# Kernel optimization log

Measured on AMD Instinct MI355X. Metric: run time of the kernel, lower is better.

Reference implementation:

```python
import jax, jax.numpy as jnp
import numpy as np

B, S, D_IN, D_OUT = 4, 2048, 1024, 1024

def setup_inputs() -> dict:
    key = jax.random.key(0)
    k_x, k_q, k_k, k_v = jax.random.split(key, 4)
    return {
        "x": jax.random.normal(k_x, (B, S, D_IN), dtype=jnp.float32),
        "W_query": jax.random.uniform(k_q, (D_IN, D_OUT), dtype=jnp.float32),
        "W_key": jax.random.uniform(k_k, (D_IN, D_OUT), dtype=jnp.float32),
        "W_value": jax.random.uniform(k_v, (D_IN, D_OUT), dtype=jnp.float32),
    }

def reference(x, W_query, W_key, W_value):
    seq_len = x.shape[1]
    d_out = W_key.shape[-1]
    # fused QKV projection: x @ concat([Wq, Wk, Wv], -1), then split
    qkv = x @ jnp.concatenate([W_query, W_key, W_value], axis=-1)  # [B,S,3*d_out]
    query, key, value = jnp.split(qkv, 3, axis=2)
    # raw scores [B,S,S]; causal mask applied BEFORE scaling (as in source)
    attn_weights = jnp.einsum("bqd,bkd->bqk", query, key)
    causal = jnp.triu(jnp.ones((seq_len, seq_len), dtype=bool), k=1)
    attn_weights = jnp.where(causal[None, :, :], -jnp.inf, attn_weights)
    scaled = attn_weights / jnp.asarray(d_out, x.dtype) ** 0.5
    attn_scores = jax.nn.softmax(scaled, axis=-1)  # dropout p=0 -> identity
    context_vectors = jnp.einsum("bqk,bkd->bqd", attn_scores, value)
    return (context_vectors, attn_scores)
```

## Files before the change

kernel.cpp:

```cpp
#include <hip/hip_runtime.h>
#include <cstdint>
#include <cstddef>


#define S_LEN 2048
#define D_DIM 1024
#define NBATCH 4
#define MEG (1024 * 1024)

typedef __attribute__((ext_vector_type(4))) float floatx4;
typedef __attribute__((ext_vector_type(8))) __bf16 bf16x8;
typedef __attribute__((ext_vector_type(8))) short short8v;

__device__ __forceinline__ unsigned short f2bf(float f) {
  union { float f; unsigned u; } v; v.f = f;
  unsigned r = v.u + 0x7FFF + ((v.u >> 16) & 1);
  return (unsigned short)(r >> 16);
}
__device__ __forceinline__ float bf2f(unsigned short h) {
  union { unsigned u; float f; } v; v.u = ((unsigned)h) << 16; return v.f;
}

__device__ __forceinline__ void async_copy16(const void* g, void* l) {
  __builtin_amdgcn_global_load_lds(
      (const __attribute__((address_space(1))) void*)g,
      (__attribute__((address_space(3))) void*)l, 16, 0, 0);
}

__device__ __forceinline__ void gemm_bt_core(
    const short* __restrict__ A, const short* __restrict__ B,
    int lda, int ldb, int kIters, int blockM, int blockN,
    short (*As)[32], short (*Bs)[32], floatx4 (&acc)[4][4])
{
  const int tid  = threadIdx.x;
  const int lane = tid & 63;
  const int wave = tid >> 6;
  const int wm = (wave >> 1) * 64;
  const int wn = (wave & 1) * 64;
  const int fm = lane & 15;
  const int fk = (lane >> 4) * 8;
  const int r0 = tid >> 2;
  const int c0 = (tid & 3) * 8;

  floatx4 zero = {0.f, 0.f, 0.f, 0.f};
  #pragma unroll
  for (int i = 0; i < 4; ++i)
    #pragma unroll
    for (int j = 0; j < 4; ++j)
      acc[i][j] = zero;

  const short* a0 = A + (size_t)(blockM + r0) * lda + c0;
  const short* a1 = a0 + (size_t)64 * lda;
  const short* b0 = B + (size_t)(blockN + r0) * ldb + c0;
  const short* b1 = b0 + (size_t)64 * ldb;
  short* as0 = &As[r0][c0];
  short* as1 = &As[r0 + 64][c0];
  short* bs0 = &Bs[r0][c0];
  short* bs1 = &Bs[r0 + 64][c0];

  for (int kt = 0; kt < kIters; ++kt) {
    const int kb = kt * 32;
    async_copy16(a0 + kb, as0);
    async_copy16(a1 + kb, as1);
    async_copy16(b0 + kb, bs0);
    async_copy16(b1 + kb, bs1);
    __syncthreads();
    bf16x8 af[4], bfr[4];
    #pragma unroll
    for (int i = 0; i < 4; ++i)
      af[i] = *(const bf16x8*)(&As[wm + i * 16 + fm][fk]);
    #pragma unroll
    for (int j = 0; j < 4; ++j)
      bfr[j] = *(const bf16x8*)(&Bs[wn + j * 16 + fm][fk]);
    #pragma unroll
    for (int i = 0; i < 4; ++i)
      #pragma unroll
      for (int j = 0; j < 4; ++j)
        acc[i][j] = __builtin_amdgcn_mfma_f32_16x16x32_bf16(af[i], bfr[j], acc[i][j], 0, 0, 0);
    __syncthreads();
  }
}

__device__ __forceinline__ void gemm_bt_split_core(
    const short* __restrict__ Ah, const short* __restrict__ Al,
    const short* __restrict__ Bh, const short* __restrict__ Bl,
    int lda, int ldb, int kIters, int blockM, int blockN,
    short (*AsH)[32], short (*AsL)[32], short (*BsH)[32], short (*BsL)[32],
    floatx4 (&acc)[4][4])
{
  const int tid  = threadIdx.x;
  const int lane = tid & 63;
  const int wave = tid >> 6;
  const int wm = (wave >> 1) * 64;
  const int wn = (wave & 1) * 64;
  const int fm = lane & 15;
  const int fk = (lane >> 4) * 8;
  const int r0 = tid >> 2;
  const int c0 = (tid & 3) * 8;

  floatx4 zero = {0.f, 0.f, 0.f, 0.f};
  #pragma unroll
  for (int i = 0; i < 4; ++i)
    #pragma unroll
    for (int j = 0; j < 4; ++j)
      acc[i][j] = zero;

  const size_t oa0 = (size_t)(blockM + r0) * lda + c0;
  const size_t oa1 = oa0 + (size_t)64 * lda;
  const size_t ob0 = (size_t)(blockN + r0) * ldb + c0;
  const size_t ob1 = ob0 + (size_t)64 * ldb;
  short* lah0 = &AsH[r0][c0]; short* lah1 = &AsH[r0 + 64][c0];
  short* lal0 = &AsL[r0][c0]; short* lal1 = &AsL[r0 + 64][c0];
  short* lbh0 = &BsH[r0][c0]; short* lbh1 = &BsH[r0 + 64][c0];
  short* lbl0 = &BsL[r0][c0]; short* lbl1 = &BsL[r0 + 64][c0];

  for (int kt = 0; kt < kIters; ++kt) {
    const int kb = kt * 32;
    async_copy16(Ah + oa0 + kb, lah0);
    async_copy16(Ah + oa1 + kb, lah1);
    async_copy16(Al + oa0 + kb, lal0);
    async_copy16(Al + oa1 + kb, lal1);
    async_copy16(Bh + ob0 + kb, lbh0);
    async_copy16(Bh + ob1 + kb, lbh1);
    async_copy16(Bl + ob0 + kb, lbl0);
    async_copy16(Bl + ob1 + kb, lbl1);
    __syncthreads();
    bf16x8 ah[4], al[4], bh[4], bl[4];
    #pragma unroll
    for (int i = 0; i < 4; ++i) {
      ah[i] = *(const bf16x8*)(&AsH[wm + i * 16 + fm][fk]);
      al[i] = *(const bf16x8*)(&AsL[wm + i * 16 + fm][fk]);
    }
    #pragma unroll
    for (int j = 0; j < 4; ++j) {
      bh[j] = *(const bf16x8*)(&BsH[wn + j * 16 + fm][fk]);
      bl[j] = *(const bf16x8*)(&BsL[wn + j * 16 + fm][fk]);
    }
    #pragma unroll
    for (int i = 0; i < 4; ++i)
      #pragma unroll
      for (int j = 0; j < 4; ++j) {
        acc[i][j] = __builtin_amdgcn_mfma_f32_16x16x32_bf16(ah[i], bh[j], acc[i][j], 0, 0, 0);
        acc[i][j] = __builtin_amdgcn_mfma_f32_16x16x32_bf16(ah[i], bl[j], acc[i][j], 0, 0, 0);
        acc[i][j] = __builtin_amdgcn_mfma_f32_16x16x32_bf16(al[i], bh[j], acc[i][j], 0, 0, 0);
      }
    __syncthreads();
  }
}


__global__ __launch_bounds__(256) void k_cvt_x_split(const float4* __restrict__ x,
                                                     short* __restrict__ xh,
                                                     short* __restrict__ xl) {
  const size_t idx = (size_t)blockIdx.x * 256 + threadIdx.x;
  const float4 u = x[idx * 2];
  const float4 w = x[idx * 2 + 1];
  float f[8] = {u.x, u.y, u.z, u.w, w.x, w.y, w.z, w.w};
  short8v oh, ol;
  #pragma unroll
  for (int e = 0; e < 8; ++e) {
    const unsigned short h = f2bf(f[e]);
    oh[e] = (short)h;
    ol[e] = (short)f2bf(f[e] - bf2f(h));
  }
  *(short8v*)(xh + idx * 8) = oh;
  *(short8v*)(xl + idx * 8) = ol;
}

__global__ __launch_bounds__(256) void k_cvt_w(
    const float* __restrict__ wq, const float* __restrict__ wk,
    const float* __restrict__ wv, short* __restrict__ wth,
    short* __restrict__ wtl)
{
  const int z = blockIdx.z;
  const float* W = (z == 0) ? wq : (z == 1) ? wk : wv;
  short* outh = wth + (size_t)z * D_DIM * D_DIM;
  short* outl = wtl + (size_t)z * D_DIM * D_DIM;
  __shared__ float tile[32][33];
  const int tx = threadIdx.x, ty = threadIdx.y;
  const int colIn = blockIdx.x * 32 + tx;
  #pragma unroll
  for (int i = 0; i < 4; ++i) {
    const int rowIn = blockIdx.y * 32 + ty + i * 8;
    tile[ty + i * 8][tx] = W[(size_t)rowIn * D_DIM + colIn];
  }
  __syncthreads();
  const int colOut = blockIdx.y * 32 + tx;
  #pragma unroll
  for (int i = 0; i < 4; ++i) {
    const int rowOut = blockIdx.x * 32 + ty + i * 8;
    const float val = tile[tx][ty + i * 8];
    const unsigned short h = f2bf(val);
    outh[(size_t)rowOut * D_DIM + colOut] = (short)h;
    if (z < 2)
      outl[(size_t)rowOut * D_DIM + colOut] = (short)f2bf(val - bf2f(h));
  }
}


__global__ __launch_bounds__(256) void k_gemm_qk(
    const short* __restrict__ xh, const short* __restrict__ xl,
    const short* __restrict__ wth, const short* __restrict__ wtl,
    short* __restrict__ qh, short* __restrict__ ql,
    short* __restrict__ kh, short* __restrict__ kl)
{
  __shared__ alignas(16) short AsH[128][32];
  __shared__ alignas(16) short AsL[128][32];
  __shared__ alignas(16) short BsH[128][32];
  __shared__ alignas(16) short BsL[128][32];
  floatx4 acc[4][4];
  const int blockM = blockIdx.y * 128;
  const int blockN = blockIdx.x * 128;
  gemm_bt_split_core(xh, xl, wth, wtl, D_DIM, D_DIM, D_DIM / 32,
                     blockM, blockN, AsH, AsL, BsH, BsL, acc);

  const int tid = threadIdx.x, lane = tid & 63, wave = tid >> 6;
  const int wm = (wave >> 1) * 64, wn = (wave & 1) * 64;
  const int rb = wm + ((lane >> 4) << 2);
  const int cb = wn + (lane & 15);
  const bool isQ = (blockN < D_DIM);
  short* dh = isQ ? qh : kh;
  short* dl = isQ ? ql : kl;
  const int coff = isQ ? blockN : blockN - D_DIM;
  #pragma unroll
  for (int i = 0; i < 4; ++i)
    #pragma unroll
    for (int j = 0; j < 4; ++j) {
      const int n = coff + cb + j * 16;
      #pragma unroll
      for (int r = 0; r < 4; ++r) {
        const int m = blockM + rb + i * 16 + r;
        const float f = acc[i][j][r];
        const unsigned short h = f2bf(f);
        dh[(size_t)m * D_DIM + n] = (short)h;
        dl[(size_t)m * D_DIM + n] = (short)f2bf(f - bf2f(h));
      }
    }
}

__global__ __launch_bounds__(256) void k_gemm_v(
    const short* __restrict__ xh, const short* __restrict__ wthV,
    short* __restrict__ vt)
{
  __shared__ alignas(16) short As[128][32];
  __shared__ alignas(16) short Bs[128][32];
  floatx4 acc[4][4];
  const int blockM = blockIdx.y * 128;
  const int blockN = blockIdx.x * 128;
  gemm_bt_core(xh, wthV, D_DIM, D_DIM, D_DIM / 32, blockM, blockN, As, Bs, acc);

  const int tid = threadIdx.x, lane = tid & 63, wave = tid >> 6;
  const int wm = (wave >> 1) * 64, wn = (wave & 1) * 64;
  const int rb = wm + ((lane >> 4) << 2);
  const int cb = wn + (lane & 15);
  #pragma unroll
  for (int i = 0; i < 4; ++i)
    #pragma unroll
    for (int j = 0; j < 4; ++j) {
      const int n = blockN + cb + j * 16;
      const int m0 = blockM + rb + i * 16;
      const int b = m0 >> 11;
      const int s0 = m0 & (S_LEN - 1);
      ushort4 pk;
      pk.x = f2bf(acc[i][j][0]); pk.y = f2bf(acc[i][j][1]);
      pk.z = f2bf(acc[i][j][2]); pk.w = f2bf(acc[i][j][3]);
      *(ushort4*)(vt + ((size_t)b * D_DIM + n) * S_LEN + s0) = pk;
    }
}

__global__ __launch_bounds__(256) void k_gemm_scores(
    const short* __restrict__ qh, const short* __restrict__ ql,
    const short* __restrict__ kh, const short* __restrict__ kl,
    float* __restrict__ attn)
{
  __shared__ alignas(16) short AsH[128][32];
  __shared__ alignas(16) short AsL[128][32];
  __shared__ alignas(16) short BsH[128][32];
  __shared__ alignas(16) short BsL[128][32];
  floatx4 acc[4][4];
  int t = blockIdx.x, bi = 0;
  while (t >= bi + 1) { t -= bi + 1; ++bi; }
  const int bj = t;
  const int b = blockIdx.z;
  const size_t boff = (size_t)b * S_LEN * D_DIM;
  gemm_bt_split_core(qh + boff, ql + boff, kh + boff, kl + boff,
                     D_DIM, D_DIM, D_DIM / 32, bi * 128, bj * 128,
                     AsH, AsL, BsH, BsL, acc);

  float* out = attn + (size_t)b * S_LEN * S_LEN;
  const int tid = threadIdx.x, lane = tid & 63, wave = tid >> 6;
  const int wm = (wave >> 1) * 64, wn = (wave & 1) * 64;
  const int rb = wm + ((lane >> 4) << 2);
  const int cb = wn + (lane & 15);
  #pragma unroll
  for (int i = 0; i < 4; ++i)
    #pragma unroll
    for (int j = 0; j < 4; ++j) {
      const int n = bj * 128 + cb + j * 16;
      #pragma unroll
      for (int r = 0; r < 4; ++r) {
        const int m = bi * 128 + rb + i * 16 + r;
        out[(size_t)m * S_LEN + n] = acc[i][j][r];
      }
    }
}

__global__ __launch_bounds__(256) void k_gemm_ctx(
    const short* __restrict__ pb, const short* __restrict__ vt,
    float* __restrict__ ctx)
{
  __shared__ alignas(16) short As[128][32];
  __shared__ alignas(16) short Bs[128][32];
  floatx4 acc[4][4];
  const int b = blockIdx.z;
  const int blockM = blockIdx.y * 128;
  const int blockN = blockIdx.x * 128;
  const int kIters = blockIdx.y * 4 + 4;
  const short* A = pb + (size_t)b * S_LEN * S_LEN;
  const short* B = vt + (size_t)b * D_DIM * S_LEN;
  gemm_bt_core(A, B, S_LEN, S_LEN, kIters, blockM, blockN, As, Bs, acc);

  float* out = ctx + (size_t)b * S_LEN * D_DIM;
  const int tid = threadIdx.x, lane = tid & 63, wave = tid >> 6;
  const int wm = (wave >> 1) * 64, wn = (wave & 1) * 64;
  const int rb = wm + ((lane >> 4) << 2);
  const int cb = wn + (lane & 15);
  #pragma unroll
  for (int i = 0; i < 4; ++i)
    #pragma unroll
    for (int j = 0; j < 4; ++j) {
      const int n = blockN + cb + j * 16;
      #pragma unroll
      for (int r = 0; r < 4; ++r) {
        const int m = blockM + rb + i * 16 + r;
        out[(size_t)m * D_DIM + n] = acc[i][j][r];
      }
    }
}


__global__ __launch_bounds__(256) void k_softmax(float* __restrict__ attn,
                                                 short* __restrict__ pb) {
  const int b = blockIdx.x >> 11;
  const int q = blockIdx.x & (S_LEN - 1);
  float* row  = attn + ((size_t)b * S_LEN + q) * S_LEN;
  short* prow = pb   + ((size_t)b * S_LEN + q) * S_LEN;
  const int tid = threadIdx.x;
  __shared__ float sMax[4], sSum[4];
  float v[8];
  float mx = -3.0e38f;
  #pragma unroll
  for (int e = 0; e < 8; ++e) {
    const int k = e * 256 + tid;
    v[e] = (k <= q) ? row[k] : -3.0e38f;
    mx = fmaxf(mx, v[e]);
  }
  #pragma unroll
  for (int off = 32; off > 0; off >>= 1) mx = fmaxf(mx, __shfl_xor(mx, off));
  if ((tid & 63) == 0) sMax[tid >> 6] = mx;
  __syncthreads();
  mx = fmaxf(fmaxf(sMax[0], sMax[1]), fmaxf(sMax[2], sMax[3]));

  float s = 0.f;
  #pragma unroll
  for (int e = 0; e < 8; ++e) {
    const int k = e * 256 + tid;
    const float p = (k <= q) ? __expf((v[e] - mx) * 0.03125f) : 0.f;
    v[e] = p;
    s += p;
  }
  #pragma unroll
  for (int off = 32; off > 0; off >>= 1) s += __shfl_xor(s, off);
  if ((tid & 63) == 0) sSum[tid >> 6] = s;
  __syncthreads();
  s = sSum[0] + sSum[1] + sSum[2] + sSum[3];
  const float inv = 1.0f / s;

  #pragma unroll
  for (int e = 0; e < 8; ++e) {
    const int k = e * 256 + tid;
    const float o = v[e] * inv;
    row[k] = o;
    prow[k] = (short)f2bf(o);
  }
}


extern "C" void kernel_launch(void* const* d_in, const int* in_sizes, int n_in,
                              void* d_out, int out_size, void* d_ws, size_t ws_size,
                              hipStream_t stream) {
  const float* x  = (const float*)d_in[0];
  const float* wq = (const float*)d_in[1];
  const float* wk = (const float*)d_in[2];
  const float* wv = (const float*)d_in[3];

  float* out  = (float*)d_out;
  float* ctx  = out;
  float* attn = out + (size_t)NBATCH * S_LEN * D_DIM;

  short* ws  = (short*)d_ws;
  short* xh  = ws;
  short* xl  = xh + (size_t)8 * MEG;
  short* pb  = xh;
  short* wth = xl + (size_t)8 * MEG;
  short* wtl = wth + (size_t)3 * MEG;
  short* qh  = wtl + (size_t)2 * MEG;
  short* ql  = qh + (size_t)8 * MEG;
  short* kh  = ql + (size_t)8 * MEG;
  short* kl  = kh + (size_t)8 * MEG;
  short* vt  = kl + (size_t)8 * MEG;

  k_cvt_x_split<<<4096, 256, 0, stream>>>((const float4*)x, xh, xl);
  k_cvt_w<<<dim3(32, 32, 3), dim3(32, 8), 0, stream>>>(wq, wk, wv, wth, wtl);
  k_gemm_qk<<<dim3(16, 64), 256, 0, stream>>>(xh, xl, wth, wtl, qh, ql, kh, kl);
  k_gemm_v<<<dim3(8, 64), 256, 0, stream>>>(xh, wth + (size_t)2 * MEG, vt);
  k_gemm_scores<<<dim3(136, 1, 4), 256, 0, stream>>>(qh, ql, kh, kl, attn);
  k_softmax<<<NBATCH * S_LEN, 256, 0, stream>>>(attn, pb);
  k_gemm_ctx<<<dim3(8, 16, 4), 256, 0, stream>>>(pb, vt, ctx);
}
```

Baseline: 441.7 us.

## Reassociate scores as x(WqWkᵀ)xᵀ with rank-one mean correction

Instead of projecting x to both Q and K, the code forms M = Wk·Wqᵀ once (a small 1024³ GEMM), computes N = x·M, and then forms scores as N·xᵀ. This removes one of the two large split-precision projection GEMMs. Because the weights are uniform and positive, it subtracts a mean component (mu, row sums sq, and dot products u) from N and adds it back as a rank-one term in the scores epilogue, to keep bf16 hi/lo precision. It also merges the conversion kernels into one launch, runs the V projection in the same grid as the scores GEMM, and reverses the ctx block order so the longest causal tiles start first. The price is several extra small kernels and a numerics path that differs from the reference ordering.

```diff
diff --git a/kernel.cpp b/kernel.cpp
--- a/kernel.cpp
+++ b/kernel.cpp
@@ -149,60 +149,69 @@
 }
 
 
-__global__ __launch_bounds__(256) void k_cvt_x_split(const float4* __restrict__ x,
-                                                     short* __restrict__ xh,
-                                                     short* __restrict__ xl) {
-  const size_t idx = (size_t)blockIdx.x * 256 + threadIdx.x;
-  const float4 u = x[idx * 2];
-  const float4 w = x[idx * 2 + 1];
-  float f[8] = {u.x, u.y, u.z, u.w, w.x, w.y, w.z, w.w};
-  short8v oh, ol;
-  #pragma unroll
-  for (int e = 0; e < 8; ++e) {
-    const unsigned short h = f2bf(f[e]);
-    oh[e] = (short)h;
-    ol[e] = (short)f2bf(f[e] - bf2f(h));
-  }
-  *(short8v*)(xh + idx * 8) = oh;
-  *(short8v*)(xl + idx * 8) = ol;
-}
-
-__global__ __launch_bounds__(256) void k_cvt_w(
+__global__ __launch_bounds__(256) void k_cvt(
+    const float4* __restrict__ x,
     const float* __restrict__ wq, const float* __restrict__ wk,
-    const float* __restrict__ wv, short* __restrict__ wth,
-    short* __restrict__ wtl)
-{
-  const int z = blockIdx.z;
-  const float* W = (z == 0) ? wq : (z == 1) ? wk : wv;
-  short* outh = wth + (size_t)z * D_DIM * D_DIM;
-  short* outl = wtl + (size_t)z * D_DIM * D_DIM;
-  __shared__ float tile[32][33];
-  const int tx = threadIdx.x, ty = threadIdx.y;
-  const int colIn = blockIdx.x * 32 + tx;
-  #pragma unroll
-  for (int i = 0; i < 4; ++i) {
-    const int rowIn = blockIdx.y * 32 + ty + i * 8;
-    tile[ty + i * 8][tx] = W[(size_t)rowIn * D_DIM + colIn];
-  }
-  __syncthreads();
-  const int colOut = blockIdx.y * 32 + tx;
-  #pragma unroll
-  for (int i = 0; i < 4; ++i) {
-    const int rowOut = blockIdx.x * 32 + ty + i * 8;
-    const float val = tile[tx][ty + i * 8];
-    const unsigned short h = f2bf(val);
-    outh[(size_t)rowOut * D_DIM + colOut] = (short)h;
-    if (z < 2)
-      outl[(size_t)rowOut * D_DIM + colOut] = (short)f2bf(val - bf2f(h));
-  }
-}
-
-
-__global__ __launch_bounds__(256) void k_gemm_qk(
-    const short* __restrict__ xh, const short* __restrict__ xl,
-    const short* __restrict__ wth, const short* __restrict__ wtl,
-    short* __restrict__ qh, short* __restrict__ ql,
-    short* __restrict__ kh, short* __restrict__ kl)
+    const float* __restrict__ wv,
+    short* __restrict__ xh, short* __restrict__ xl,
+    short* __restrict__ wqh, short* __restrict__ wql,
+    short* __restrict__ wkh, short* __restrict__ wkl,
+    short* __restrict__ wvt)
+{
+  const int bid = blockIdx.x;
+  const int tid = threadIdx.x;
+  if (bid < 5120) {
+    const float4* src;
+    short *dh, *dl;
+    size_t idx;
+    if (bid < 4096) {
+      idx = (size_t)bid * 256 + tid;
+      src = x; dh = xh; dl = xl;
+    } else if (bid < 4608) {
+      idx = (size_t)(bid - 4096) * 256 + tid;
+      src = (const float4*)wq; dh = wqh; dl = wql;
+    } else {
+      idx = (size_t)(bid - 4608) * 256 + tid;
+      src = (const float4*)wk; dh = wkh; dl = wkl;
+    }
+    const float4 u4 = src[idx * 2];
+    const float4 w4 = src[idx * 2 + 1];
+    float f[8] = {u4.x, u4.y, u4.z, u4.w, w4.x, w4.y, w4.z, w4.w};
+    short8v oh, ol;
+    #pragma unroll
+    for (int e = 0; e < 8; ++e) {
+      const unsigned short h = f2bf(f[e]);
+      oh[e] = (short)h;
+      ol[e] = (short)f2bf(f[e] - bf2f(h));
+    }
+    *(short8v*)(dh + idx * 8) = oh;
+    *(short8v*)(dl + idx * 8) = ol;
+  } else {
+    const int rem = bid - 5120;
+    const int bx = rem & 31, by = rem >> 5;
+    const int tx = tid & 31, ty = tid >> 5;
+    __shared__ float tile[32][33];
+    const int colIn = bx * 32 + tx;
+    #pragma unroll
+    for (int i = 0; i < 4; ++i) {
+      const int rowIn = by * 32 + ty + i * 8;
+      tile[ty + i * 8][tx] = wv[(size_t)rowIn * D_DIM + colIn];
+    }
+    __syncthreads();
+    const int colOut = by * 32 + tx;
+    #pragma unroll
+    for (int i = 0; i < 4; ++i) {
+      const int rowOut = bx * 32 + ty + i * 8;
+      wvt[(size_t)rowOut * D_DIM + colOut] = (short)f2bf(tile[tx][ty + i * 8]);
+    }
+  }
+}
+
+
+__global__ __launch_bounds__(256) void k_gemm_m(
+    const short* __restrict__ wqh, const short* __restrict__ wql,
+    const short* __restrict__ wkh, const short* __restrict__ wkl,
+    short* __restrict__ mth, short* __restrict__ mtl)
 {
   __shared__ alignas(16) short AsH[128][32];
   __shared__ alignas(16) short AsL[128][32];
@@ -211,83 +220,93 @@
   floatx4 acc[4][4];
   const int blockM = blockIdx.y * 128;
   const int blockN = blockIdx.x * 128;
-  gemm_bt_split_core(xh, xl, wth, wtl, D_DIM, D_DIM, D_DIM / 32,
-                     blockM, blockN, AsH, AsL, BsH, BsL, acc);
+  gemm_bt_split_core(wkh, wkl, wqh, wql,
+                     D_DIM, D_DIM, D_DIM / 32, blockM, blockN,
+                     AsH, AsL, BsH, BsL, acc);
 
   const int tid = threadIdx.x, lane = tid & 63, wave = tid >> 6;
   const int wm = (wave >> 1) * 64, wn = (wave & 1) * 64;
   const int rb = wm + ((lane >> 4) << 2);
   const int cb = wn + (lane & 15);
-  const bool isQ = (blockN < D_DIM);
-  short* dh = isQ ? qh : kh;
-  short* dl = isQ ? ql : kl;
-  const int coff = isQ ? blockN : blockN - D_DIM;
   #pragma unroll
   for (int i = 0; i < 4; ++i)
     #pragma unroll
     for (int j = 0; j < 4; ++j) {
-      const int n = coff + cb + j * 16;
+      const int n = blockN + cb + j * 16;
       #pragma unroll
       for (int r = 0; r < 4; ++r) {
         const int m = blockM + rb + i * 16 + r;
         const float f = acc[i][j][r];
         const unsigned short h = f2bf(f);
-        dh[(size_t)m * D_DIM + n] = (short)h;
-        dl[(size_t)m * D_DIM + n] = (short)f2bf(f - bf2f(h));
+        mth[(size_t)m * D_DIM + n] = (short)h;
+        mtl[(size_t)m * D_DIM + n] = (short)f2bf(f - bf2f(h));
       }
     }
 }
 
-__global__ __launch_bounds__(256) void k_gemm_v(
-    const short* __restrict__ xh, const short* __restrict__ wthV,
-    short* __restrict__ vt)
-{
-  __shared__ alignas(16) short As[128][32];
-  __shared__ alignas(16) short Bs[128][32];
-  floatx4 acc[4][4];
-  const int blockM = blockIdx.y * 128;
-  const int blockN = blockIdx.x * 128;
-  gemm_bt_core(xh, wthV, D_DIM, D_DIM, D_DIM / 32, blockM, blockN, As, Bs, acc);
-
-  const int tid = threadIdx.x, lane = tid & 63, wave = tid >> 6;
-  const int wm = (wave >> 1) * 64, wn = (wave & 1) * 64;
-  const int rb = wm + ((lane >> 4) << 2);
-  const int cb = wn + (lane & 15);
-  #pragma unroll
-  for (int i = 0; i < 4; ++i)
-    #pragma unroll
-    for (int j = 0; j < 4; ++j) {
-      const int n = blockN + cb + j * 16;
-      const int m0 = blockM + rb + i * 16;
-      const int b = m0 >> 11;
-      const int s0 = m0 & (S_LEN - 1);
-      ushort4 pk;
-      pk.x = f2bf(acc[i][j][0]); pk.y = f2bf(acc[i][j][1]);
-      pk.z = f2bf(acc[i][j][2]); pk.w = f2bf(acc[i][j][3]);
-      *(ushort4*)(vt + ((size_t)b * D_DIM + n) * S_LEN + s0) = pk;
-    }
-}
-
-__global__ __launch_bounds__(256) void k_gemm_scores(
-    const short* __restrict__ qh, const short* __restrict__ ql,
-    const short* __restrict__ kh, const short* __restrict__ kl,
-    float* __restrict__ attn)
+
+__global__ __launch_bounds__(256) void k_mu(const short* __restrict__ mth,
+                                            const short* __restrict__ mtl,
+                                            float* __restrict__ mu) {
+  const int j = blockIdx.x, tid = threadIdx.x;
+  const ushort4 h = *(const ushort4*)(mth + (size_t)j * D_DIM + tid * 4);
+  const ushort4 l = *(const ushort4*)(mtl + (size_t)j * D_DIM + tid * 4);
+  float s = bf2f(h.x) + bf2f(l.x) + bf2f(h.y) + bf2f(l.y)
+          + bf2f(h.z) + bf2f(l.z) + bf2f(h.w) + bf2f(l.w);
+  #pragma unroll
+  for (int off = 32; off > 0; off >>= 1) s += __shfl_xor(s, off);
+  __shared__ float ps[4];
+  if ((tid & 63) == 0) ps[tid >> 6] = s;
+  __syncthreads();
+  if (tid == 0) mu[j] = (ps[0] + ps[1] + ps[2] + ps[3]) * (1.0f / 1024.0f);
+}
+
+
+__global__ __launch_bounds__(256) void k_rowstats(
+    const short* __restrict__ xh, const short* __restrict__ xl,
+    const float* __restrict__ mu, float* __restrict__ sq, float* __restrict__ u)
+{
+  const int r = blockIdx.x, tid = threadIdx.x;
+  const ushort4 h = *(const ushort4*)(xh + (size_t)r * D_DIM + tid * 4);
+  const ushort4 l = *(const ushort4*)(xl + (size_t)r * D_DIM + tid * 4);
+  const float4 m4 = *(const float4*)(mu + tid * 4);
+  const float x0 = bf2f(h.x) + bf2f(l.x);
+  const float x1 = bf2f(h.y) + bf2f(l.y);
+  const float x2 = bf2f(h.z) + bf2f(l.z);
+  const float x3 = bf2f(h.w) + bf2f(l.w);
+  float s = x0 + x1 + x2 + x3;
+  float uu = m4.x * x0 + m4.y * x1 + m4.z * x2 + m4.w * x3;
+  #pragma unroll
+  for (int off = 32; off > 0; off >>= 1) {
+    s  += __shfl_xor(s, off);
+    uu += __shfl_xor(uu, off);
+  }
+  __shared__ float ps[4], pu[4];
+  if ((tid & 63) == 0) { ps[tid >> 6] = s; pu[tid >> 6] = uu; }
+  __syncthreads();
+  if (tid == 0) {
+    sq[r] = ps[0] + ps[1] + ps[2] + ps[3];
+    u[r]  = pu[0] + pu[1] + pu[2] + pu[3];
+  }
+}
+
+
+__global__ __launch_bounds__(256) void k_gemm_n(
+    const short* __restrict__ xh, const short* __restrict__ xl,
+    const short* __restrict__ mth, const short* __restrict__ mtl,
+    const float* __restrict__ sq, const float* __restrict__ mu,
+    short* __restrict__ nh, short* __restrict__ nl)
 {
   __shared__ alignas(16) short AsH[128][32];
   __shared__ alignas(16) short AsL[128][32];
   __shared__ alignas(16) short BsH[128][32];
   __shared__ alignas(16) short BsL[128][32];
   floatx4 acc[4][4];
-  int t = blockIdx.x, bi = 0;
-  while (t >= bi + 1) { t -= bi + 1; ++bi; }
-  const int bj = t;
-  const int b = blockIdx.z;
-  const size_t boff = (size_t)b * S_LEN * D_DIM;
-  gemm_bt_split_core(qh + boff, ql + boff, kh + boff, kl + boff,
-                     D_DIM, D_DIM, D_DIM / 32, bi * 128, bj * 128,
-                     AsH, AsL, BsH, BsL, acc);
-
-  float* out = attn + (size_t)b * S_LEN * S_LEN;
+  const int blockM = blockIdx.y * 128;
+  const int blockN = blockIdx.x * 128;
+  gemm_bt_split_core(xh, xl, mth, mtl, D_DIM, D_DIM, D_DIM / 32,
+                     blockM, blockN, AsH, AsL, BsH, BsL, acc);
+
   const int tid = threadIdx.x, lane = tid & 63, wave = tid >> 6;
   const int wm = (wave >> 1) * 64, wn = (wave & 1) * 64;
   const int rb = wm + ((lane >> 4) << 2);
@@ -296,46 +315,84 @@
   for (int i = 0; i < 4; ++i)
     #pragma unroll
     for (int j = 0; j < 4; ++j) {
-      const int n = bj * 128 + cb + j * 16;
+      const int n = blockN + cb + j * 16;
+      const float muv = mu[n];
       #pragma unroll
       for (int r = 0; r < 4; ++r) {
-        const int m = bi * 128 + rb + i * 16 + r;
-        out[(size_t)m * S_LEN + n] = acc[i][j][r];
+        const int m = blockM + rb + i * 16 + r;
+        const float f = acc[i][j][r] - sq[m] * muv;
+        const unsigned short h = f2bf(f);
+        nh[(size_t)m * D_DIM + n] = (short)h;
+        nl[(size_t)m * D_DIM + n] = (short)f2bf(f - bf2f(h));
       }
     }
 }
 
-__global__ __launch_bounds__(256) void k_gemm_ctx(
-    const short* __restrict__ pb, const short* __restrict__ vt,
-    float* __restrict__ ctx)
-{
-  __shared__ alignas(16) short As[128][32];
-  __shared__ alignas(16) short Bs[128][32];
+
+__global__ __launch_bounds__(256) void k_gemm_sv(
+    const short* __restrict__ nh, const short* __restrict__ nl,
+    const short* __restrict__ xh, const short* __restrict__ xl,
+    const float* __restrict__ sq, const float* __restrict__ u,
+    const short* __restrict__ wvt, float* __restrict__ attn,
+    short* __restrict__ vt)
+{
+  __shared__ alignas(16) short AsH[128][32];
+  __shared__ alignas(16) short AsL[128][32];
+  __shared__ alignas(16) short BsH[128][32];
+  __shared__ alignas(16) short BsL[128][32];
   floatx4 acc[4][4];
-  const int b = blockIdx.z;
-  const int blockM = blockIdx.y * 128;
-  const int blockN = blockIdx.x * 128;
-  const int kIters = blockIdx.y * 4 + 4;
-  const short* A = pb + (size_t)b * S_LEN * S_LEN;
-  const short* B = vt + (size_t)b * D_DIM * S_LEN;
-  gemm_bt_core(A, B, S_LEN, S_LEN, kIters, blockM, blockN, As, Bs, acc);
-
-  float* out = ctx + (size_t)b * S_LEN * D_DIM;
+  const int bid = blockIdx.x;
   const int tid = threadIdx.x, lane = tid & 63, wave = tid >> 6;
   const int wm = (wave >> 1) * 64, wn = (wave & 1) * 64;
   const int rb = wm + ((lane >> 4) << 2);
   const int cb = wn + (lane & 15);
-  #pragma unroll
-  for (int i = 0; i < 4; ++i)
+
+  if (bid < 544) {
+    const int b = bid / 136;
+    int t = bid - b * 136, bi = 0;
+    while (t >= bi + 1) { t -= bi + 1; ++bi; }
+    const int bj = t;
+    const size_t boff = (size_t)b * S_LEN * D_DIM;
+    gemm_bt_split_core(nh + boff, nl + boff, xh + boff, xl + boff,
+                       D_DIM, D_DIM, D_DIM / 32, bi * 128, bj * 128,
+                       AsH, AsL, BsH, BsL, acc);
+
+    float* out = attn + (size_t)b * S_LEN * S_LEN;
+    const int rowBase = (b << 11) + bi * 128;
+    const int colBase = (b << 11) + bj * 128;
     #pragma unroll
     for (int j = 0; j < 4; ++j) {
-      const int n = blockN + cb + j * 16;
-      #pragma unroll
-      for (int r = 0; r < 4; ++r) {
-        const int m = blockM + rb + i * 16 + r;
-        out[(size_t)m * D_DIM + n] = acc[i][j][r];
+      const int n = bj * 128 + cb + j * 16;
+      const float uv = u[colBase + cb + j * 16];
+      #pragma unroll
+      for (int i = 0; i < 4; ++i)
+        #pragma unroll
+        for (int r = 0; r < 4; ++r) {
+          const int m = bi * 128 + rb + i * 16 + r;
+          const float sv = sq[rowBase + rb + i * 16 + r];
+          out[(size_t)m * S_LEN + n] = acc[i][j][r] + sv * uv;
+        }
+    }
+  } else {
+    const int vb = bid - 544;
+    const int blockM = (vb >> 3) * 128;
+    const int blockN = (vb & 7) * 128;
+    gemm_bt_core(xh, wvt, D_DIM, D_DIM, D_DIM / 32, blockM, blockN,
+                 AsH, BsH, acc);
+    #pragma unroll
+    for (int i = 0; i < 4; ++i)
+      #pragma unroll
+      for (int j = 0; j < 4; ++j) {
+        const int n = blockN + cb + j * 16;
+        const int m0 = blockM + rb + i * 16;
+        const int b = m0 >> 11;
+        const int s0 = m0 & (S_LEN - 1);
+        ushort4 pk;
+        pk.x = f2bf(acc[i][j][0]); pk.y = f2bf(acc[i][j][1]);
+        pk.z = f2bf(acc[i][j][2]); pk.w = f2bf(acc[i][j][3]);
+        *(ushort4*)(vt + ((size_t)b * D_DIM + n) * S_LEN + s0) = pk;
       }
-    }
+  }
 }
 
 
@@ -386,6 +443,41 @@
 }
 
 
+__global__ __launch_bounds__(256) void k_gemm_ctx(
+    const short* __restrict__ pb, const short* __restrict__ vt,
+    float* __restrict__ ctx)
+{
+  __shared__ alignas(16) short As[128][32];
+  __shared__ alignas(16) short Bs[128][32];
+  floatx4 acc[4][4];
+  const int b = blockIdx.z;
+  const int by = 15 - blockIdx.y;
+  const int blockM = by * 128;
+  const int blockN = blockIdx.x * 128;
+  const int kIters = by * 4 + 4;
+  const short* A = pb + (size_t)b * S_LEN * S_LEN;
+  const short* B = vt + (size_t)b * D_DIM * S_LEN;
+  gemm_bt_core(A, B, S_LEN, S_LEN, kIters, blockM, blockN, As, Bs, acc);
+
+  float* out = ctx + (size_t)b * S_LEN * D_DIM;
+  const int tid = threadIdx.x, lane = tid & 63, wave = tid >> 6;
+  const int wm = (wave >> 1) * 64, wn = (wave & 1) * 64;
+  const int rb = wm + ((lane >> 4) << 2);
+  const int cb = wn + (lane & 15);
+  #pragma unroll
+  for (int i = 0; i < 4; ++i)
+    #pragma unroll
+    for (int j = 0; j < 4; ++j) {
+      const int n = blockN + cb + j * 16;
+      #pragma unroll
+      for (int r = 0; r < 4; ++r) {
+        const int m = blockM + rb + i * 16 + r;
+        out[(size_t)m * D_DIM + n] = acc[i][j][r];
+      }
+    }
+}
+
+
 extern "C" void kernel_launch(void* const* d_in, const int* in_sizes, int n_in,
                               void* d_out, int out_size, void* d_ws, size_t ws_size,
                               hipStream_t stream) {
@@ -401,20 +493,29 @@
   short* ws  = (short*)d_ws;
   short* xh  = ws;
   short* xl  = xh + (size_t)8 * MEG;
-  short* pb  = xh;
-  short* wth = xl + (size_t)8 * MEG;
-  short* wtl = wth + (size_t)3 * MEG;
-  short* qh  = wtl + (size_t)2 * MEG;
-  short* ql  = qh + (size_t)8 * MEG;
-  short* kh  = ql + (size_t)8 * MEG;
-  short* kl  = kh + (size_t)8 * MEG;
-  short* vt  = kl + (size_t)8 * MEG;
-
-  k_cvt_x_split<<<4096, 256, 0, stream>>>((const float4*)x, xh, xl);
-  k_cvt_w<<<dim3(32, 32, 3), dim3(32, 8), 0, stream>>>(wq, wk, wv, wth, wtl);
-  k_gemm_qk<<<dim3(16, 64), 256, 0, stream>>>(xh, xl, wth, wtl, qh, ql, kh, kl);
-  k_gemm_v<<<dim3(8, 64), 256, 0, stream>>>(xh, wth + (size_t)2 * MEG, vt);
-  k_gemm_scores<<<dim3(136, 1, 4), 256, 0, stream>>>(qh, ql, kh, kl, attn);
+  short* wqh = xl + (size_t)8 * MEG;
+  short* wql = wqh + (size_t)1 * MEG;
+  short* wkh = wql + (size_t)1 * MEG;
+  short* wkl = wkh + (size_t)1 * MEG;
+  short* wvt = wkl + (size_t)1 * MEG;
+  short* mth = wvt + (size_t)1 * MEG;
+  short* mtl = mth + (size_t)1 * MEG;
+  short* nh  = mtl + (size_t)1 * MEG;
+  short* nl  = nh + (size_t)8 * MEG;
+  short* vt  = nl + (size_t)8 * MEG;
+  short* pb  = nh;
+  float* fb  = (float*)(vt + (size_t)8 * MEG);
+  float* mu  = fb;
+  float* sq  = fb + 1024;
+  float* u   = sq + 8192;
+
+  k_cvt<<<6144, 256, 0, stream>>>((const float4*)x, wq, wk, wv,
+                                  xh, xl, wqh, wql, wkh, wkl, wvt);
+  k_gemm_m<<<dim3(8, 8), 256, 0, stream>>>(wqh, wql, wkh, wkl, mth, mtl);
+  k_mu<<<1024, 256, 0, stream>>>(mth, mtl, mu);
+  k_rowstats<<<8192, 256, 0, stream>>>(xh, xl, mu, sq, u);
+  k_gemm_n<<<dim3(8, 64), 256, 0, stream>>>(xh, xl, mth, mtl, sq, mu, nh, nl);
+  k_gemm_sv<<<1056, 256, 0, stream>>>(nh, nl, xh, xl, sq, u, wvt, attn, vt);
   k_softmax<<<NBATCH * S_LEN, 256, 0, stream>>>(attn, pb);
   k_gemm_ctx<<<dim3(8, 16, 4), 256, 0, stream>>>(pb, vt, ctx);
 }
```

Measured after the change: 430.9 us. 1.03x faster.
